# Performance work log

Measured on AMD Instinct MI355X. Metric: run time of the kernel, lower is better.

Reference implementation:

```python
import jax, jax.numpy as jnp
import numpy as np

N_NODES = 100000
N_EDGES = 1600000
D_IN = 64
D_HID = 64
NEG_SLOPE = 0.01  # torch leaky_relu default


def _sage_conv(x, src, dst, W_l, b_l, W_r):
    # PyG SAGEConv (mean aggr): lin_l(mean_j x_j) + lin_r(x_i)
    n = x.shape[0]
    msg = x[src]  # [E, D] irregular gather
    agg = jax.ops.segment_sum(msg, dst, num_segments=n)
    deg = jax.ops.segment_sum(jnp.ones((src.shape[0],), x.dtype), dst, num_segments=n)
    mean = agg / jnp.maximum(deg, 1.0)[:, None]
    return mean @ W_l.T + b_l + x @ W_r.T


def setup_inputs() -> dict:
    key = jax.random.key(0)
    ks = jax.random.split(key, 12)
    x = jax.random.normal(ks[0], (N_NODES, D_IN), dtype=jnp.float32)
    edge_index = jax.random.randint(ks[1], (2, N_EDGES), 0, N_NODES, dtype=jnp.int64)
    s = 1.0 / np.sqrt(D_IN)
    params = {}
    dims = [(D_IN, D_HID), (D_HID, D_HID), (D_HID, D_HID)]
    ki = 2
    for i, (din, dout) in enumerate(dims, start=1):
        sc = 1.0 / np.sqrt(din)
        params[f'W_l{i}'] = jax.random.uniform(ks[ki], (dout, din), minval=-sc, maxval=sc, dtype=jnp.float32); ki += 1
        params[f'b_l{i}'] = jnp.zeros((dout,), jnp.float32)
        params[f'W_r{i}'] = jax.random.uniform(ks[ki], (dout, din), minval=-sc, maxval=sc, dtype=jnp.float32); ki += 1
    sc = 1.0 / np.sqrt(D_HID)
    params['W_out'] = jax.random.uniform(ks[ki], (1, D_HID), minval=-sc, maxval=sc, dtype=jnp.float32)
    params['b_out'] = jnp.zeros((1,), jnp.float32)
    return {'x': x, 'edge_index': edge_index, **params}


def reference(x, edge_index, W_l1, b_l1, W_r1, W_l2, b_l2, W_r2, W_l3, b_l3, W_r3, W_out, b_out):
    src, dst = edge_index[0], edge_index[1]
    h = x
    for (Wl, bl, Wr) in ((W_l1, b_l1, W_r1), (W_l2, b_l2, W_r2), (W_l3, b_l3, W_r3)):
        h = _sage_conv(h, src, dst, Wl, bl, Wr)
        h = jnp.where(h >= 0, h, NEG_SLOPE * h)
        # dropout is identity in eval mode
    return h @ W_out.T + b_out  # [N, 1]
```

## Files before the change

### kernel.cpp

```cpp
#include <hip/hip_runtime.h>
#include <hip/hip_fp16.h>

#define D 64
#define NEG_SLOPE 0.01f
#define CB_SHIFT 9
#define CB_NODES 512
#define MAXCB 256
#define CHUNK 4096
#define BCAP 10240
#define SADJ_CAP 10240
#define CGRID 256
#define SAH 72
#define TILE 64

typedef _Float16 f16x8 __attribute__((ext_vector_type(8)));
typedef float    f32x4 __attribute__((ext_vector_type(4)));

struct ScatSmem {
    int hist[MAXCB];
    int lofs[MAXCB];
    int gbase[MAXCB];
    int cur[MAXCB];
    int swsum[4];
    unsigned spk[CHUNK];
    unsigned char sbk[CHUNK];
};

__device__ __forceinline__ int detect64(const void* __restrict__ ei) {
    int lane = threadIdx.x & 63;
    int v = ((const int*)ei)[2 * lane + 1];
    return (__ballot(v != 0) == 0ULL) ? 1 : 0;
}

__device__ __forceinline__ int edge_at(const void* __restrict__ ei, long long idx, int is64) {
    if (is64) return (int)((const long long*)ei)[idx];
    return ((const int*)ei)[idx];
}

__device__ __forceinline__ void scatter_body(ScatSmem& sm,
        const void* __restrict__ ei, long long E,
        int* __restrict__ bcursor, unsigned* __restrict__ ebuf,
        int ncb, int bid) {
    int t = threadIdx.x;
    sm.hist[t] = 0;
    int is64 = detect64(ei);
    __syncthreads();
    long long start = (long long)bid * CHUNK;
    int ccnt = (int)min((long long)CHUNK, E - start);

    for (int i = t; i < ccnt; i += 256) {
        int d = edge_at(ei, E + start + i, is64);
        atomicAdd(&sm.hist[d >> CB_SHIFT], 1);
    }
    __syncthreads();
    {
        int v = sm.hist[t];
        int lane = t & 63, w = t >> 6;
        int inc = v;
        for (int off = 1; off < 64; off <<= 1) {
            int u = __shfl_up(inc, off, 64);
            if (lane >= off) inc += u;
        }
        if (lane == 63) sm.swsum[w] = inc;
        __syncthreads();
        int wof = 0;
        for (int i = 0; i < w; ++i) wof += sm.swsum[i];
        sm.lofs[t] = wof + inc - v;
    }
    if (t < ncb && sm.hist[t]) sm.gbase[t] = atomicAdd(&bcursor[t], sm.hist[t]);
    __syncthreads();
    sm.cur[t] = sm.lofs[t];
    __syncthreads();

    for (int i = t; i < ccnt; i += 256) {
        int s = edge_at(ei, start + i, is64);
        int d = edge_at(ei, E + start + i, is64);
        int b = d >> CB_SHIFT;
        int slot = atomicAdd(&sm.cur[b], 1);
        sm.spk[slot] = ((unsigned)s << CB_SHIFT) | (unsigned)(d & (CB_NODES - 1));
        sm.sbk[slot] = (unsigned char)b;
    }
    __syncthreads();

    for (int i = t; i < ccnt; i += 256) {
        int b = sm.sbk[i];
        int dst = sm.gbase[b] + (i - sm.lofs[b]);
        if (dst < BCAP) ebuf[(size_t)b * BCAP + dst] = sm.spk[i];
    }
}

__device__ __forceinline__ void conv_body(const float* __restrict__ x,
        _Float16* __restrict__ x16, long long U, int cid,
        const float* __restrict__ Wl1, const float* __restrict__ Wr1,
        const float* __restrict__ Wl2, const float* __restrict__ Wr2,
        const float* __restrict__ Wl3, const float* __restrict__ Wr3,
        _Float16* __restrict__ W16) {
    int t = threadIdx.x;
    for (long long u = (long long)cid * 256 + t; u < U; u += (long long)CGRID * 256) {
        const float* s = x + u * 8;
        const float4 v0 = *(const float4*)s;
        const float4 v1 = *(const float4*)(s + 4);
        f16x8 o = { (_Float16)v0.x, (_Float16)v0.y, (_Float16)v0.z, (_Float16)v0.w,
                    (_Float16)v1.x, (_Float16)v1.y, (_Float16)v1.z, (_Float16)v1.w };
        *(f16x8*)(x16 + u * 8) = o;
    }
    if (cid == 0) {
        const float* Ws[6] = { Wl1, Wr1, Wl2, Wr2, Wl3, Wr3 };
#pragma unroll
        for (int m = 0; m < 6; ++m) {
            const float* src = Ws[m];
            _Float16* dst = W16 + m * 4096;
            for (int i = t; i < 4096; i += 256) dst[i] = (_Float16)src[i];
        }
    }
}

__global__ __launch_bounds__(256, 6) void scatter_conv_kernel(
        const void* __restrict__ ei, long long E,
        int* __restrict__ bcursor, unsigned* __restrict__ ebuf, int ncb, int sgrid,
        const float* __restrict__ x, _Float16* __restrict__ x16, long long U,
        const float* __restrict__ Wl1, const float* __restrict__ Wr1,
        const float* __restrict__ Wl2, const float* __restrict__ Wr2,
        const float* __restrict__ Wl3, const float* __restrict__ Wr3,
        _Float16* __restrict__ W16) {
    __shared__ ScatSmem sm;
    if ((int)blockIdx.x < sgrid)
        scatter_body(sm, ei, E, bcursor, ebuf, ncb, blockIdx.x);
    else
        conv_body(x, x16, U, blockIdx.x - sgrid, Wl1, Wr1, Wl2, Wr2, Wl3, Wr3, W16);
}

__global__ __launch_bounds__(256) void agg_gemm_kernel(
        const _Float16* __restrict__ Hin,
        const int* __restrict__ rowptr, const int* __restrict__ adj,
        const _Float16* __restrict__ W16,
        const float* __restrict__ bl,
        _Float16* __restrict__ Hout,
        const float* __restrict__ Wout, const float* __restrict__ bout,
        float* __restrict__ out, int N, int final_flag) {
    __shared__ _Float16 smh[TILE * SAH];
    int t = threadIdx.x;
    int node_base = (int)blockIdx.x * TILE;

    {
        int g = t >> 3;
        int sub = t & 7;
        size_t cofs = (size_t)(sub << 3);
#pragma unroll
        for (int p = 0; p < 2; ++p) {
            int local = p * 32 + g;
            int i = node_base + local;
            float a0 = 0.f, a1 = 0.f, a2 = 0.f, a3 = 0.f;
            float a4 = 0.f, a5 = 0.f, a6 = 0.f, a7 = 0.f;
            float inv = 0.f;
            if (i < N) {
                int b0 = rowptr[i], b1 = rowptr[i + 1];
                int e = b0;
                int nfull = (b1 - b0) >> 2;
                for (int q = 0; q < nfull; ++q) {
                    int s0 = adj[e], s1 = adj[e + 1], s2 = adj[e + 2], s3 = adj[e + 3];
                    e += 4;
                    union { float4 f4; __half2 h2[4]; } u0, u1, u2, u3;
                    u0.f4 = *(const float4*)(Hin + (size_t)s0 * D + cofs);
                    u1.f4 = *(const float4*)(Hin + (size_t)s1 * D + cofs);
                    u2.f4 = *(const float4*)(Hin + (size_t)s2 * D + cofs);
                    u3.f4 = *(const float4*)(Hin + (size_t)s3 * D + cofs);
#define ACC8(u) { \
        float2 v0 = __half22float2(u.h2[0]); float2 v1 = __half22float2(u.h2[1]); \
        float2 v2 = __half22float2(u.h2[2]); float2 v3 = __half22float2(u.h2[3]); \
        a0 += v0.x; a1 += v0.y; a2 += v1.x; a3 += v1.y; \
        a4 += v2.x; a5 += v2.y; a6 += v3.x; a7 += v3.y; }
                    ACC8(u0) ACC8(u1) ACC8(u2) ACC8(u3)
                }
                for (; e < b1; ++e) {
                    int s = adj[e];
                    union { float4 f4; __half2 h2[4]; } u;
                    u.f4 = *(const float4*)(Hin + (size_t)s * D + cofs);
                    ACC8(u)
                }
#undef ACC8
                inv = 1.0f / fmaxf((float)(b1 - b0), 1.0f);
            }
            f16x8 o = { (_Float16)(a0 * inv), (_Float16)(a1 * inv),
                        (_Float16)(a2 * inv), (_Float16)(a3 * inv),
                        (_Float16)(a4 * inv), (_Float16)(a5 * inv),
                        (_Float16)(a6 * inv), (_Float16)(a7 * inv) };
            *(f16x8*)(smh + local * SAH + (sub << 3)) = o;
        }
    }
    __syncthreads();

    int w = t >> 6, lane = t & 63;
    int lr = lane & 15;
    int lk = lane >> 4;
    int rbase = node_base + w * 16;

    f16x8 ah[2], am[2];
    {
        int gn = rbase + lr;
        if (gn >= N) gn = N - 1;
        const _Float16* hp = Hin + (size_t)gn * D + lk * 8;
        ah[0] = *(const f16x8*)hp;  ah[1] = *(const f16x8*)(hp + 32);
        const _Float16* mp = smh + (w * 16 + lr) * SAH + lk * 8;
        am[0] = *(const f16x8*)mp;  am[1] = *(const f16x8*)(mp + 32);
    }

    f32x4 acc[4];
#pragma unroll
    for (int nt = 0; nt < 4; ++nt)
        acc[nt] = (f32x4){0.f, 0.f, 0.f, 0.f};

    const _Float16* Wl = W16;
    const _Float16* Wr = W16 + 4096;
#pragma unroll
    for (int nt = 0; nt < 4; ++nt) {
        const _Float16* pl = Wl + (nt * 16 + lr) * D + lk * 8;
        const _Float16* pr = Wr + (nt * 16 + lr) * D + lk * 8;
        f16x8 b0 = *(const f16x8*)pl;  f16x8 b1 = *(const f16x8*)(pl + 32);
        f16x8 c0 = *(const f16x8*)pr;  f16x8 c1 = *(const f16x8*)(pr + 32);
        acc[nt] = __builtin_amdgcn_mfma_f32_16x16x32_f16(am[0], b0, acc[nt], 0, 0, 0);
        acc[nt] = __builtin_amdgcn_mfma_f32_16x16x32_f16(am[1], b1, acc[nt], 0, 0, 0);
        acc[nt] = __builtin_amdgcn_mfma_f32_16x16x32_f16(ah[0], c0, acc[nt], 0, 0, 0);
        acc[nt] = __builtin_amdgcn_mfma_f32_16x16x32_f16(ah[1], c1, acc[nt], 0, 0, 0);
    }

    float blv[4];
#pragma unroll
    for (int nt = 0; nt < 4; ++nt) blv[nt] = bl[nt * 16 + lr];

    if (!final_flag) {
#pragma unroll
        for (int r = 0; r < 4; ++r) {
            int gn = rbase + lk * 4 + r;
            if (gn < N) {
#pragma unroll
                for (int nt = 0; nt < 4; ++nt) {
                    float y = acc[nt][r] + blv[nt];
                    y = (y >= 0.f) ? y : NEG_SLOPE * y;
                    Hout[(size_t)gn * D + nt * 16 + lr] = (_Float16)y;
                }
            }
        }
    } else {
        float wv[4];
#pragma unroll
        for (int nt = 0; nt < 4; ++nt) wv[nt] = Wout[nt * 16 + lr];
        float bo = bout[0];
#pragma unroll
        for (int r = 0; r < 4; ++r) {
            float p = 0.f;
#pragma unroll
            for (int nt = 0; nt < 4; ++nt) {
                float y = acc[nt][r] + blv[nt];
                y = (y >= 0.f) ? y : NEG_SLOPE * y;
                p += y * wv[nt];
            }
            p += __shfl_xor(p, 1, 64);
            p += __shfl_xor(p, 2, 64);
            p += __shfl_xor(p, 4, 64);
            p += __shfl_xor(p, 8, 64);
            int gn = rbase + lk * 4 + r;
            if (lr == 0 && gn < N) out[gn] = p + bo;
        }
    }
}

__global__ __launch_bounds__(256) void finefill_kernel(
        const unsigned* __restrict__ ebuf, const int* __restrict__ bcount,
        int* __restrict__ rowptr, int* __restrict__ adj, int N, int ncb) {
    __shared__ int cnt[CB_NODES];
    __shared__ int cur[CB_NODES];
    __shared__ int wpart[4];
    __shared__ int wsum4[4];
    __shared__ int se0;
    __shared__ int sAdj[SADJ_CAP];
    int t = threadIdx.x;
    int b = blockIdx.x;

    {
        int v = (t < ncb) ? min(bcount[t], BCAP) : 0;
        int lane = t & 63, w = t >> 6;
        int inc = v;
        for (int off = 1; off < 64; off <<= 1) {
            int u = __shfl_up(inc, off, 64);
            if (lane >= off) inc += u;
        }
        if (lane == 63) wsum4[w] = inc;
        __syncthreads();
        int wof = 0;
        for (int iw = 0; iw < w; ++iw) wof += wsum4[iw];
        int ex = wof + inc - v;
        if (t == b) se0 = ex;
        if (b == 0 && t == 0)
            rowptr[N] = wsum4[0] + wsum4[1] + wsum4[2] + wsum4[3];
    }
    __syncthreads();
    int e0 = se0;
    int len = min(bcount[b], BCAP);
    int nb = b << CB_SHIFT;
    const unsigned* slab = ebuf + (size_t)b * BCAP;

    cnt[2 * t] = 0; cnt[2 * t + 1] = 0;
    __syncthreads();
    for (int i = t; i < len; i += 256) {
        unsigned p = slab[i];
        atomicAdd(&cnt[p & (CB_NODES - 1)], 1);
    }
    __syncthreads();

    int c0 = cnt[2 * t], c1 = cnt[2 * t + 1];
    int s = c0 + c1;
    int lane = t & 63, wv = t >> 6;
    int inc = s;
    for (int off = 1; off < 64; off <<= 1) {
        int u = __shfl_up(inc, off, 64);
        if (lane >= off) inc += u;
    }
    if (lane == 63) wpart[wv] = inc;
    __syncthreads();
    int wof = 0;
    for (int w = 0; w < wv; ++w) wof += wpart[w];
    int ex = wof + inc - s;
    cur[2 * t] = ex; cur[2 * t + 1] = ex + c0;
    {
        int g = nb + 2 * t;
        if (g < N)     rowptr[g]     = e0 + ex;
        if (g + 1 < N) rowptr[g + 1] = e0 + ex + c0;
    }
    __syncthreads();

    int big = (len > SADJ_CAP);
    for (int i = t; i < len; i += 256) {
        unsigned p = slab[i];
        int dl = (int)(p & (CB_NODES - 1));
        int src = (int)(p >> CB_SHIFT);
        int pos = atomicAdd(&cur[dl], 1);
        if (big) adj[e0 + pos] = src;
        else     sAdj[pos] = src;
    }
    __syncthreads();
    if (!big) {
        for (int i = t; i < len; i += 256) adj[e0 + i] = sAdj[i];
    }
}

extern "C" void kernel_launch(void* const* d_in, const int* in_sizes, int n_in,
                              void* d_out, int out_size, void* d_ws, size_t ws_size,
                              hipStream_t stream) {
    const float* x    = (const float*)d_in[0];
    const void*  ei   = d_in[1];
    const float* Wl1  = (const float*)d_in[2];
    const float* bl1  = (const float*)d_in[3];
    const float* Wr1  = (const float*)d_in[4];
    const float* Wl2  = (const float*)d_in[5];
    const float* bl2  = (const float*)d_in[6];
    const float* Wr2  = (const float*)d_in[7];
    const float* Wl3  = (const float*)d_in[8];
    const float* bl3  = (const float*)d_in[9];
    const float* Wr3  = (const float*)d_in[10];
    const float* Wout = (const float*)d_in[11];
    const float* bout = (const float*)d_in[12];
    float* out = (float*)d_out;

    int       N = in_sizes[0] / D;
    long long E = (long long)in_sizes[1] / 2;
    int ncb = (N + CB_NODES - 1) >> CB_SHIFT;
    long long U = (long long)N * D / 8;

    char* ws = (char*)d_ws;
    size_t off = 256;
    int* bcursor = (int*)(ws + off); off += 1024;
    int* rowptr = (int*)(ws + off); off += (((size_t)(N + 1) * 4 + 255) / 256) * 256;
    int* adj    = (int*)(ws + off); off += (((size_t)E * 4 + 255) / 256) * 256;
    unsigned* ebuf = (unsigned*)(ws + off); off += (size_t)ncb * BCAP * 4;
    _Float16* x16 = (_Float16*)(ws + off); off += (size_t)N * D * 2;
    _Float16* hA  = (_Float16*)(ws + off); off += (size_t)N * D * 2;
    _Float16* hB  = (_Float16*)(ws + off); off += (size_t)N * D * 2;
    _Float16* W16 = (_Float16*)(ws + off); off += 6 * 4096 * 2;

    int sgrid = (int)((E + CHUNK - 1) / CHUNK);
    int ggrid = (N + TILE - 1) / TILE;

    hipMemsetAsync(bcursor, 0, 1024, stream);

    scatter_conv_kernel<<<sgrid + CGRID, 256, 0, stream>>>(
        ei, E, bcursor, ebuf, ncb, sgrid,
        x, x16, U, Wl1, Wr1, Wl2, Wr2, Wl3, Wr3, W16);
    finefill_kernel<<<ncb, 256, 0, stream>>>(ebuf, bcursor, rowptr, adj, N, ncb);
    agg_gemm_kernel<<<ggrid, 256, 0, stream>>>(x16, rowptr, adj, W16, bl1, hA,
                                               Wout, bout, out, N, 0);
    agg_gemm_kernel<<<ggrid, 256, 0, stream>>>(hA, rowptr, adj, W16 + 2 * 4096, bl2, hB,
                                               Wout, bout, out, N, 0);
    agg_gemm_kernel<<<ggrid, 256, 0, stream>>>(hB, rowptr, adj, W16 + 4 * 4096, bl3, hA,
                                               Wout, bout, out, N, 1);
}
```

Baseline: 260.4 us.

## Replace two-pass bucketed CSR build with fixed-capacity per-node adjacency via atomics

```diff
diff --git a/kernel.cpp b/kernel.cpp
--- a/kernel.cpp
+++ b/kernel.cpp
@@ -3,28 +3,13 @@
 
 #define D 64
 #define NEG_SLOPE 0.01f
-#define CB_SHIFT 9
-#define CB_NODES 512
-#define MAXCB 256
-#define CHUNK 4096
-#define BCAP 10240
-#define SADJ_CAP 10240
-#define CGRID 256
+#define CAP 64
 #define SAH 72
 #define TILE 64
+#define BGRID 2048
 
 typedef _Float16 f16x8 __attribute__((ext_vector_type(8)));
 typedef float    f32x4 __attribute__((ext_vector_type(4)));
-
-struct ScatSmem {
-    int hist[MAXCB];
-    int lofs[MAXCB];
-    int gbase[MAXCB];
-    int cur[MAXCB];
-    int swsum[4];
-    unsigned spk[CHUNK];
-    unsigned char sbk[CHUNK];
-};
 
 __device__ __forceinline__ int detect64(const void* __restrict__ ei) {
     int lane = threadIdx.x & 63;
@@ -37,66 +22,25 @@
     return ((const int*)ei)[idx];
 }
 
-__device__ __forceinline__ void scatter_body(ScatSmem& sm,
+__global__ __launch_bounds__(256) void build_kernel(
         const void* __restrict__ ei, long long E,
-        int* __restrict__ bcursor, unsigned* __restrict__ ebuf,
-        int ncb, int bid) {
-    int t = threadIdx.x;
-    sm.hist[t] = 0;
-    int is64 = detect64(ei);
-    __syncthreads();
-    long long start = (long long)bid * CHUNK;
-    int ccnt = (int)min((long long)CHUNK, E - start);
-
-    for (int i = t; i < ccnt; i += 256) {
-        int d = edge_at(ei, E + start + i, is64);
-        atomicAdd(&sm.hist[d >> CB_SHIFT], 1);
-    }
-    __syncthreads();
-    {
-        int v = sm.hist[t];
-        int lane = t & 63, w = t >> 6;
-        int inc = v;
-        for (int off = 1; off < 64; off <<= 1) {
-            int u = __shfl_up(inc, off, 64);
-            if (lane >= off) inc += u;
-        }
-        if (lane == 63) sm.swsum[w] = inc;
-        __syncthreads();
-        int wof = 0;
-        for (int i = 0; i < w; ++i) wof += sm.swsum[i];
-        sm.lofs[t] = wof + inc - v;
-    }
-    if (t < ncb && sm.hist[t]) sm.gbase[t] = atomicAdd(&bcursor[t], sm.hist[t]);
-    __syncthreads();
-    sm.cur[t] = sm.lofs[t];
-    __syncthreads();
-
-    for (int i = t; i < ccnt; i += 256) {
-        int s = edge_at(ei, start + i, is64);
-        int d = edge_at(ei, E + start + i, is64);
-        int b = d >> CB_SHIFT;
-        int slot = atomicAdd(&sm.cur[b], 1);
-        sm.spk[slot] = ((unsigned)s << CB_SHIFT) | (unsigned)(d & (CB_NODES - 1));
-        sm.sbk[slot] = (unsigned char)b;
-    }
-    __syncthreads();
-
-    for (int i = t; i < ccnt; i += 256) {
-        int b = sm.sbk[i];
-        int dst = sm.gbase[b] + (i - sm.lofs[b]);
-        if (dst < BCAP) ebuf[(size_t)b * BCAP + dst] = sm.spk[i];
-    }
-}
-
-__device__ __forceinline__ void conv_body(const float* __restrict__ x,
-        _Float16* __restrict__ x16, long long U, int cid,
+        int* __restrict__ deg, int* __restrict__ adjF,
+        const float* __restrict__ x, _Float16* __restrict__ x16, long long U,
         const float* __restrict__ Wl1, const float* __restrict__ Wr1,
         const float* __restrict__ Wl2, const float* __restrict__ Wr2,
         const float* __restrict__ Wl3, const float* __restrict__ Wr3,
         _Float16* __restrict__ W16) {
-    int t = threadIdx.x;
-    for (long long u = (long long)cid * 256 + t; u < U; u += (long long)CGRID * 256) {
+    long long tid = (long long)blockIdx.x * 256 + threadIdx.x;
+    long long stride = (long long)gridDim.x * 256;
+    int is64 = detect64(ei);
+
+    for (long long e = tid; e < E; e += stride) {
+        int s = edge_at(ei, e, is64);
+        int d = edge_at(ei, E + e, is64);
+        int pos = atomicAdd(&deg[d], 1);
+        if (pos < CAP) adjF[(size_t)d * CAP + pos] = s;
+    }
+    for (long long u = tid; u < U; u += stride) {
         const float* s = x + u * 8;
         const float4 v0 = *(const float4*)s;
         const float4 v1 = *(const float4*)(s + 4);
@@ -104,8 +48,9 @@
                     (_Float16)v1.x, (_Float16)v1.y, (_Float16)v1.z, (_Float16)v1.w };
         *(f16x8*)(x16 + u * 8) = o;
     }
-    if (cid == 0) {
+    if (blockIdx.x == 0) {
         const float* Ws[6] = { Wl1, Wr1, Wl2, Wr2, Wl3, Wr3 };
+        int t = threadIdx.x;
 #pragma unroll
         for (int m = 0; m < 6; ++m) {
             const float* src = Ws[m];
@@ -115,24 +60,9 @@
     }
 }
 
-__global__ __launch_bounds__(256, 6) void scatter_conv_kernel(
-        const void* __restrict__ ei, long long E,
-        int* __restrict__ bcursor, unsigned* __restrict__ ebuf, int ncb, int sgrid,
-        const float* __restrict__ x, _Float16* __restrict__ x16, long long U,
-        const float* __restrict__ Wl1, const float* __restrict__ Wr1,
-        const float* __restrict__ Wl2, const float* __restrict__ Wr2,
-        const float* __restrict__ Wl3, const float* __restrict__ Wr3,
-        _Float16* __restrict__ W16) {
-    __shared__ ScatSmem sm;
-    if ((int)blockIdx.x < sgrid)
-        scatter_body(sm, ei, E, bcursor, ebuf, ncb, blockIdx.x);
-    else
-        conv_body(x, x16, U, blockIdx.x - sgrid, Wl1, Wr1, Wl2, Wr2, Wl3, Wr3, W16);
-}
-
 __global__ __launch_bounds__(256) void agg_gemm_kernel(
         const _Float16* __restrict__ Hin,
-        const int* __restrict__ rowptr, const int* __restrict__ adj,
+        const int* __restrict__ deg, const int* __restrict__ adjF,
         const _Float16* __restrict__ W16,
         const float* __restrict__ bl,
         _Float16* __restrict__ Hout,
@@ -154,11 +84,13 @@
             float a4 = 0.f, a5 = 0.f, a6 = 0.f, a7 = 0.f;
             float inv = 0.f;
             if (i < N) {
-                int b0 = rowptr[i], b1 = rowptr[i + 1];
-                int e = b0;
-                int nfull = (b1 - b0) >> 2;
+                int dgf = deg[i];
+                int len = min(dgf, CAP);
+                const int* ap = adjF + (size_t)i * CAP;
+                int e = 0;
+                int nfull = len >> 2;
                 for (int q = 0; q < nfull; ++q) {
-                    int s0 = adj[e], s1 = adj[e + 1], s2 = adj[e + 2], s3 = adj[e + 3];
+                    int s0 = ap[e], s1 = ap[e + 1], s2 = ap[e + 2], s3 = ap[e + 3];
                     e += 4;
                     union { float4 f4; __half2 h2[4]; } u0, u1, u2, u3;
                     u0.f4 = *(const float4*)(Hin + (size_t)s0 * D + cofs);
@@ -172,14 +104,14 @@
         a4 += v2.x; a5 += v2.y; a6 += v3.x; a7 += v3.y; }
                     ACC8(u0) ACC8(u1) ACC8(u2) ACC8(u3)
                 }
-                for (; e < b1; ++e) {
-                    int s = adj[e];
+                for (; e < len; ++e) {
+                    int s = ap[e];
                     union { float4 f4; __half2 h2[4]; } u;
                     u.f4 = *(const float4*)(Hin + (size_t)s * D + cofs);
                     ACC8(u)
                 }
 #undef ACC8
-                inv = 1.0f / fmaxf((float)(b1 - b0), 1.0f);
+                inv = 1.0f / fmaxf((float)dgf, 1.0f);
             }
             f16x8 o = { (_Float16)(a0 * inv), (_Float16)(a1 * inv),
                         (_Float16)(a2 * inv), (_Float16)(a3 * inv),
@@ -262,85 +194,6 @@
             int gn = rbase + lk * 4 + r;
             if (lr == 0 && gn < N) out[gn] = p + bo;
         }
-    }
-}
-
-__global__ __launch_bounds__(256) void finefill_kernel(
-        const unsigned* __restrict__ ebuf, const int* __restrict__ bcount,
-        int* __restrict__ rowptr, int* __restrict__ adj, int N, int ncb) {
-    __shared__ int cnt[CB_NODES];
-    __shared__ int cur[CB_NODES];
-    __shared__ int wpart[4];
-    __shared__ int wsum4[4];
-    __shared__ int se0;
-    __shared__ int sAdj[SADJ_CAP];
-    int t = threadIdx.x;
-    int b = blockIdx.x;
-
-    {
-        int v = (t < ncb) ? min(bcount[t], BCAP) : 0;
-        int lane = t & 63, w = t >> 6;
-        int inc = v;
-        for (int off = 1; off < 64; off <<= 1) {
-            int u = __shfl_up(inc, off, 64);
-            if (lane >= off) inc += u;
-        }
-        if (lane == 63) wsum4[w] = inc;
-        __syncthreads();
-        int wof = 0;
-        for (int iw = 0; iw < w; ++iw) wof += wsum4[iw];
-        int ex = wof + inc - v;
-        if (t == b) se0 = ex;
-        if (b == 0 && t == 0)
-            rowptr[N] = wsum4[0] + wsum4[1] + wsum4[2] + wsum4[3];
-    }
-    __syncthreads();
-    int e0 = se0;
-    int len = min(bcount[b], BCAP);
-    int nb = b << CB_SHIFT;
-    const unsigned* slab = ebuf + (size_t)b * BCAP;
-
-    cnt[2 * t] = 0; cnt[2 * t + 1] = 0;
-    __syncthreads();
-    for (int i = t; i < len; i += 256) {
-        unsigned p = slab[i];
-        atomicAdd(&cnt[p & (CB_NODES - 1)], 1);
-    }
-    __syncthreads();
-
-    int c0 = cnt[2 * t], c1 = cnt[2 * t + 1];
-    int s = c0 + c1;
-    int lane = t & 63, wv = t >> 6;
-    int inc = s;
-    for (int off = 1; off < 64; off <<= 1) {
-        int u = __shfl_up(inc, off, 64);
-        if (lane >= off) inc += u;
-    }
-    if (lane == 63) wpart[wv] = inc;
-    __syncthreads();
-    int wof = 0;
-    for (int w = 0; w < wv; ++w) wof += wpart[w];
-    int ex = wof + inc - s;
-    cur[2 * t] = ex; cur[2 * t + 1] = ex + c0;
-    {
-        int g = nb + 2 * t;
-        if (g < N)     rowptr[g]     = e0 + ex;
-        if (g + 1 < N) rowptr[g + 1] = e0 + ex + c0;
-    }
-    __syncthreads();
-
-    int big = (len > SADJ_CAP);
-    for (int i = t; i < len; i += 256) {
-        unsigned p = slab[i];
-        int dl = (int)(p & (CB_NODES - 1));
-        int src = (int)(p >> CB_SHIFT);
-        int pos = atomicAdd(&cur[dl], 1);
-        if (big) adj[e0 + pos] = src;
-        else     sAdj[pos] = src;
-    }
-    __syncthreads();
-    if (!big) {
-        for (int i = t; i < len; i += 256) adj[e0 + i] = sAdj[i];
     }
 }
 
@@ -364,33 +217,28 @@
 
     int       N = in_sizes[0] / D;
     long long E = (long long)in_sizes[1] / 2;
-    int ncb = (N + CB_NODES - 1) >> CB_SHIFT;
     long long U = (long long)N * D / 8;
 
     char* ws = (char*)d_ws;
     size_t off = 256;
-    int* bcursor = (int*)(ws + off); off += 1024;
-    int* rowptr = (int*)(ws + off); off += (((size_t)(N + 1) * 4 + 255) / 256) * 256;
-    int* adj    = (int*)(ws + off); off += (((size_t)E * 4 + 255) / 256) * 256;
-    unsigned* ebuf = (unsigned*)(ws + off); off += (size_t)ncb * BCAP * 4;
+    int* deg  = (int*)(ws + off); off += (((size_t)N * 4 + 255) / 256) * 256;
+    int* adjF = (int*)(ws + off); off += (size_t)N * CAP * 4;
     _Float16* x16 = (_Float16*)(ws + off); off += (size_t)N * D * 2;
     _Float16* hA  = (_Float16*)(ws + off); off += (size_t)N * D * 2;
     _Float16* hB  = (_Float16*)(ws + off); off += (size_t)N * D * 2;
     _Float16* W16 = (_Float16*)(ws + off); off += 6 * 4096 * 2;
 
-    int sgrid = (int)((E + CHUNK - 1) / CHUNK);
     int ggrid = (N + TILE - 1) / TILE;
 
-    hipMemsetAsync(bcursor, 0, 1024, stream);
-
-    scatter_conv_kernel<<<sgrid + CGRID, 256, 0, stream>>>(
-        ei, E, bcursor, ebuf, ncb, sgrid,
-        x, x16, U, Wl1, Wr1, Wl2, Wr2, Wl3, Wr3, W16);
-    finefill_kernel<<<ncb, 256, 0, stream>>>(ebuf, bcursor, rowptr, adj, N, ncb);
-    agg_gemm_kernel<<<ggrid, 256, 0, stream>>>(x16, rowptr, adj, W16, bl1, hA,
+    hipMemsetAsync(deg, 0, (size_t)N * 4, stream);
+
+    build_kernel<<<BGRID, 256, 0, stream>>>(
+        ei, E, deg, adjF, x, x16, U,
+        Wl1, Wr1, Wl2, Wr2, Wl3, Wr3, W16);
+    agg_gemm_kernel<<<ggrid, 256, 0, stream>>>(x16, deg, adjF, W16, bl1, hA,
                                                Wout, bout, out, N, 0);
-    agg_gemm_kernel<<<ggrid, 256, 0, stream>>>(hA, rowptr, adj, W16 + 2 * 4096, bl2, hB,
+    agg_gemm_kernel<<<ggrid, 256, 0, stream>>>(hA, deg, adjF, W16 + 2 * 4096, bl2, hB,
                                                Wout, bout, out, N, 0);
-    agg_gemm_kernel<<<ggrid, 256, 0, stream>>>(hB, rowptr, adj, W16 + 4 * 4096, bl3, hA,
+    agg_gemm_kernel<<<ggrid, 256, 0, stream>>>(hB, deg, adjF, W16 + 4 * 4096, bl3, hA,
                                                Wout, bout, out, N, 1);
 }
```

After: 338.9 us. +30.1%, slower.

## Shrink coarse buckets to 128 nodes so CSR fill uses more blocks

Applied to the files above, without the earlier changes.

```diff
diff --git a/kernel.cpp b/kernel.cpp
--- a/kernel.cpp
+++ b/kernel.cpp
@@ -3,12 +3,11 @@
 
 #define D 64
 #define NEG_SLOPE 0.01f
-#define CB_SHIFT 9
-#define CB_NODES 512
-#define MAXCB 256
+#define CB_SHIFT 7
+#define CB_NODES 128
+#define MAXCB 1024
 #define CHUNK 4096
-#define BCAP 10240
-#define SADJ_CAP 10240
+#define BCAP 2560
 #define CGRID 256
 #define SAH 72
 #define TILE 64
@@ -23,7 +22,7 @@
     int cur[MAXCB];
     int swsum[4];
     unsigned spk[CHUNK];
-    unsigned char sbk[CHUNK];
+    unsigned short sbk[CHUNK];
 };
 
 __device__ __forceinline__ int detect64(const void* __restrict__ ei) {
@@ -42,7 +41,8 @@
         int* __restrict__ bcursor, unsigned* __restrict__ ebuf,
         int ncb, int bid) {
     int t = threadIdx.x;
-    sm.hist[t] = 0;
+#pragma unroll
+    for (int q = 0; q < 4; ++q) sm.hist[q * 256 + t] = 0;
     int is64 = detect64(ei);
     __syncthreads();
     long long start = (long long)bid * CHUNK;
@@ -54,7 +54,9 @@
     }
     __syncthreads();
     {
-        int v = sm.hist[t];
+        int h0 = sm.hist[4 * t], h1 = sm.hist[4 * t + 1];
+        int h2 = sm.hist[4 * t + 2], h3 = sm.hist[4 * t + 3];
+        int v = h0 + h1 + h2 + h3;
         int lane = t & 63, w = t >> 6;
         int inc = v;
         for (int off = 1; off < 64; off <<= 1) {
@@ -65,11 +67,19 @@
         __syncthreads();
         int wof = 0;
         for (int i = 0; i < w; ++i) wof += sm.swsum[i];
-        sm.lofs[t] = wof + inc - v;
-    }
-    if (t < ncb && sm.hist[t]) sm.gbase[t] = atomicAdd(&bcursor[t], sm.hist[t]);
-    __syncthreads();
-    sm.cur[t] = sm.lofs[t];
+        int ex = wof + inc - v;
+        sm.lofs[4 * t]     = ex;
+        sm.lofs[4 * t + 1] = ex + h0;
+        sm.lofs[4 * t + 2] = ex + h0 + h1;
+        sm.lofs[4 * t + 3] = ex + h0 + h1 + h2;
+#pragma unroll
+        for (int q = 0; q < 4; ++q) {
+            int b = 4 * t + q;
+            int hv = sm.hist[b];
+            if (b < ncb && hv) sm.gbase[b] = atomicAdd(&bcursor[b], hv);
+            sm.cur[b] = sm.lofs[b];
+        }
+    }
     __syncthreads();
 
     for (int i = t; i < ccnt; i += 256) {
@@ -78,7 +88,7 @@
         int b = d >> CB_SHIFT;
         int slot = atomicAdd(&sm.cur[b], 1);
         sm.spk[slot] = ((unsigned)s << CB_SHIFT) | (unsigned)(d & (CB_NODES - 1));
-        sm.sbk[slot] = (unsigned char)b;
+        sm.sbk[slot] = (unsigned short)b;
     }
     __syncthreads();
 
@@ -115,7 +125,7 @@
     }
 }
 
-__global__ __launch_bounds__(256, 6) void scatter_conv_kernel(
+__global__ __launch_bounds__(256, 3) void scatter_conv_kernel(
         const void* __restrict__ ei, long long E,
         int* __restrict__ bcursor, unsigned* __restrict__ ebuf, int ncb, int sgrid,
         const float* __restrict__ x, _Float16* __restrict__ x16, long long U,
@@ -128,6 +138,89 @@
         scatter_body(sm, ei, E, bcursor, ebuf, ncb, blockIdx.x);
     else
         conv_body(x, x16, U, blockIdx.x - sgrid, Wl1, Wr1, Wl2, Wr2, Wl3, Wr3, W16);
+}
+
+__global__ __launch_bounds__(256) void finefill_kernel(
+        const unsigned* __restrict__ ebuf, const int* __restrict__ bcount,
+        int* __restrict__ rowptr, int* __restrict__ adj, int N, int ncb) {
+    __shared__ int cnt[CB_NODES];
+    __shared__ int cur[CB_NODES];
+    __shared__ int wsum4[4];
+    __shared__ int se0;
+    __shared__ int sAdj[BCAP];
+    int t = threadIdx.x;
+    int b = blockIdx.x;
+
+    {
+        int b0 = 4 * t;
+        int v0 = (b0 + 0 < ncb) ? min(bcount[b0 + 0], BCAP) : 0;
+        int v1 = (b0 + 1 < ncb) ? min(bcount[b0 + 1], BCAP) : 0;
+        int v2 = (b0 + 2 < ncb) ? min(bcount[b0 + 2], BCAP) : 0;
+        int v3 = (b0 + 3 < ncb) ? min(bcount[b0 + 3], BCAP) : 0;
+        int s = v0 + v1 + v2 + v3;
+        int lane = t & 63, w = t >> 6;
+        int inc = s;
+        for (int off = 1; off < 64; off <<= 1) {
+            int u = __shfl_up(inc, off, 64);
+            if (lane >= off) inc += u;
+        }
+        if (lane == 63) wsum4[w] = inc;
+        __syncthreads();
+        int wof = 0;
+        for (int iw = 0; iw < w; ++iw) wof += wsum4[iw];
+        int ex = wof + inc - s;
+        if (b0 <= b && b < b0 + 4) {
+            int e = ex;
+            if (b > b0)     e += v0;
+            if (b > b0 + 1) e += v1;
+            if (b > b0 + 2) e += v2;
+            se0 = e;
+        }
+        if (b == 0 && t == 0)
+            rowptr[N] = wsum4[0] + wsum4[1] + wsum4[2] + wsum4[3];
+    }
+    __syncthreads();
+    int e0 = se0;
+    int len = min(bcount[b], BCAP);
+    int nb = b << CB_SHIFT;
+    const unsigned* slab = ebuf + (size_t)b * BCAP;
+
+    if (t < CB_NODES) cnt[t] = 0;
+    __syncthreads();
+    for (int i = t; i < len; i += 256)
+        atomicAdd(&cnt[slab[i] & (CB_NODES - 1)], 1);
+    __syncthreads();
+
+    {
+        int v = (t < CB_NODES) ? cnt[t] : 0;
+        int lane = t & 63, w = t >> 6;
+        int inc = v;
+        for (int off = 1; off < 64; off <<= 1) {
+            int u = __shfl_up(inc, off, 64);
+            if (lane >= off) inc += u;
+        }
+        if (lane == 63) wsum4[w] = inc;
+        __syncthreads();
+        int wof = 0;
+        for (int iw = 0; iw < w; ++iw) wof += wsum4[iw];
+        int ex = wof + inc - v;
+        if (t < CB_NODES) {
+            cur[t] = ex;
+            int g = nb + t;
+            if (g < N) rowptr[g] = e0 + ex;
+        }
+    }
+    __syncthreads();
+
+    for (int i = t; i < len; i += 256) {
+        unsigned p = slab[i];
+        int dl = (int)(p & (CB_NODES - 1));
+        int src = (int)(p >> CB_SHIFT);
+        int pos = atomicAdd(&cur[dl], 1);
+        sAdj[pos] = src;
+    }
+    __syncthreads();
+    for (int i = t; i < len; i += 256) adj[e0 + i] = sAdj[i];
 }
 
 __global__ __launch_bounds__(256) void agg_gemm_kernel(
@@ -265,85 +358,6 @@
     }
 }
 
-__global__ __launch_bounds__(256) void finefill_kernel(
-        const unsigned* __restrict__ ebuf, const int* __restrict__ bcount,
-        int* __restrict__ rowptr, int* __restrict__ adj, int N, int ncb) {
-    __shared__ int cnt[CB_NODES];
-    __shared__ int cur[CB_NODES];
-    __shared__ int wpart[4];
-    __shared__ int wsum4[4];
-    __shared__ int se0;
-    __shared__ int sAdj[SADJ_CAP];
-    int t = threadIdx.x;
-    int b = blockIdx.x;
-
-    {
-        int v = (t < ncb) ? min(bcount[t], BCAP) : 0;
-        int lane = t & 63, w = t >> 6;
-        int inc = v;
-        for (int off = 1; off < 64; off <<= 1) {
-            int u = __shfl_up(inc, off, 64);
-            if (lane >= off) inc += u;
-        }
-        if (lane == 63) wsum4[w] = inc;
-        __syncthreads();
-        int wof = 0;
-        for (int iw = 0; iw < w; ++iw) wof += wsum4[iw];
-        int ex = wof + inc - v;
-        if (t == b) se0 = ex;
-        if (b == 0 && t == 0)
-            rowptr[N] = wsum4[0] + wsum4[1] + wsum4[2] + wsum4[3];
-    }
-    __syncthreads();
-    int e0 = se0;
-    int len = min(bcount[b], BCAP);
-    int nb = b << CB_SHIFT;
-    const unsigned* slab = ebuf + (size_t)b * BCAP;
-
-    cnt[2 * t] = 0; cnt[2 * t + 1] = 0;
-    __syncthreads();
-    for (int i = t; i < len; i += 256) {
-        unsigned p = slab[i];
-        atomicAdd(&cnt[p & (CB_NODES - 1)], 1);
-    }
-    __syncthreads();
-
-    int c0 = cnt[2 * t], c1 = cnt[2 * t + 1];
-    int s = c0 + c1;
-    int lane = t & 63, wv = t >> 6;
-    int inc = s;
-    for (int off = 1; off < 64; off <<= 1) {
-        int u = __shfl_up(inc, off, 64);
-        if (lane >= off) inc += u;
-    }
-    if (lane == 63) wpart[wv] = inc;
-    __syncthreads();
-    int wof = 0;
-    for (int w = 0; w < wv; ++w) wof += wpart[w];
-    int ex = wof + inc - s;
-    cur[2 * t] = ex; cur[2 * t + 1] = ex + c0;
-    {
-        int g = nb + 2 * t;
-        if (g < N)     rowptr[g]     = e0 + ex;
-        if (g + 1 < N) rowptr[g + 1] = e0 + ex + c0;
-    }
-    __syncthreads();
-
-    int big = (len > SADJ_CAP);
-    for (int i = t; i < len; i += 256) {
-        unsigned p = slab[i];
-        int dl = (int)(p & (CB_NODES - 1));
-        int src = (int)(p >> CB_SHIFT);
-        int pos = atomicAdd(&cur[dl], 1);
-        if (big) adj[e0 + pos] = src;
-        else     sAdj[pos] = src;
-    }
-    __syncthreads();
-    if (!big) {
-        for (int i = t; i < len; i += 256) adj[e0 + i] = sAdj[i];
-    }
-}
-
 extern "C" void kernel_launch(void* const* d_in, const int* in_sizes, int n_in,
                               void* d_out, int out_size, void* d_ws, size_t ws_size,
                               hipStream_t stream) {
@@ -369,7 +383,7 @@
 
     char* ws = (char*)d_ws;
     size_t off = 256;
-    int* bcursor = (int*)(ws + off); off += 1024;
+    int* bcursor = (int*)(ws + off); off += 4096;
     int* rowptr = (int*)(ws + off); off += (((size_t)(N + 1) * 4 + 255) / 256) * 256;
     int* adj    = (int*)(ws + off); off += (((size_t)E * 4 + 255) / 256) * 256;
     unsigned* ebuf = (unsigned*)(ws + off); off += (size_t)ncb * BCAP * 4;
@@ -381,7 +395,7 @@
     int sgrid = (int)((E + CHUNK - 1) / CHUNK);
     int ggrid = (N + TILE - 1) / TILE;
 
-    hipMemsetAsync(bcursor, 0, 1024, stream);
+    hipMemsetAsync(bcursor, 0, 4096, stream);
 
     scatter_conv_kernel<<<sgrid + CGRID, 256, 0, stream>>>(
         ei, E, bcursor, ebuf, ncb, sgrid,
```

After: 274.4 us. 1.05x slower.

## Split finefill CSR build into four blocks per coarse bucket by node quarter

Applied to the files above, without the earlier changes.

```diff
diff --git a/kernel.cpp b/kernel.cpp
--- a/kernel.cpp
+++ b/kernel.cpp
@@ -8,7 +8,7 @@
 #define MAXCB 256
 #define CHUNK 4096
 #define BCAP 10240
-#define SADJ_CAP 10240
+#define QCAP 3072
 #define CGRID 256
 #define SAH 72
 #define TILE 64
@@ -128,6 +128,86 @@
         scatter_body(sm, ei, E, bcursor, ebuf, ncb, blockIdx.x);
     else
         conv_body(x, x16, U, blockIdx.x - sgrid, Wl1, Wr1, Wl2, Wr2, Wl3, Wr3, W16);
+}
+
+__global__ __launch_bounds__(256) void finefill_kernel(
+        const unsigned* __restrict__ ebuf, const int* __restrict__ bcount,
+        int* __restrict__ rowptr, int* __restrict__ adj, int N, int ncb) {
+    __shared__ int cnt[CB_NODES];
+    __shared__ int cur[CB_NODES];
+    __shared__ int wsum4[4];
+    __shared__ int se0;
+    __shared__ int sAdj[QCAP];
+    int t = threadIdx.x;
+    int B = (int)blockIdx.x >> 2;
+    int q = (int)blockIdx.x & 3;
+
+    {
+        int v = (t < ncb) ? min(bcount[t], BCAP) : 0;
+        int lane = t & 63, w = t >> 6;
+        int inc = v;
+        for (int off = 1; off < 64; off <<= 1) {
+            int u = __shfl_up(inc, off, 64);
+            if (lane >= off) inc += u;
+        }
+        if (lane == 63) wsum4[w] = inc;
+        __syncthreads();
+        int wof = 0;
+        for (int iw = 0; iw < w; ++iw) wof += wsum4[iw];
+        int ex = wof + inc - v;
+        if (t == B) se0 = ex;
+        if (blockIdx.x == 0 && t == 0)
+            rowptr[N] = wsum4[0] + wsum4[1] + wsum4[2] + wsum4[3];
+    }
+    __syncthreads();
+    int e0 = se0;
+    int len = min(bcount[B], BCAP);
+    int nb = B << CB_SHIFT;
+    const unsigned* slab = ebuf + (size_t)B * BCAP;
+
+    cnt[2 * t] = 0; cnt[2 * t + 1] = 0;
+    __syncthreads();
+    for (int i = t; i < len; i += 256)
+        atomicAdd(&cnt[slab[i] & (CB_NODES - 1)], 1);
+    __syncthreads();
+
+    {
+        int c0 = cnt[2 * t], c1 = cnt[2 * t + 1];
+        int s = c0 + c1;
+        int lane = t & 63, wv = t >> 6;
+        int inc = s;
+        for (int off = 1; off < 64; off <<= 1) {
+            int u = __shfl_up(inc, off, 64);
+            if (lane >= off) inc += u;
+        }
+        if (lane == 63) wsum4[wv] = inc;
+        __syncthreads();
+        int wof = 0;
+        for (int w = 0; w < wv; ++w) wof += wsum4[w];
+        int ex = wof + inc - s;
+        cur[2 * t] = ex; cur[2 * t + 1] = ex + c0;
+        int g = nb + 2 * t;
+        if (g < N)     rowptr[g]     = e0 + ex;
+        if (g + 1 < N) rowptr[g + 1] = e0 + ex + c0;
+    }
+    __syncthreads();
+
+    int qbase = cur[q * 128];
+    int qend  = (q < 3) ? cur[q * 128 + 128] : len;
+    int qlen  = qend - qbase;
+    __syncthreads();
+
+    for (int i = t; i < len; i += 256) {
+        unsigned p = slab[i];
+        int dl = (int)(p & (CB_NODES - 1));
+        if ((dl >> 7) == q) {
+            int pos = atomicAdd(&cur[dl], 1) - qbase;
+            if (pos < QCAP) sAdj[pos] = (int)(p >> CB_SHIFT);
+        }
+    }
+    __syncthreads();
+    for (int i = t; i < qlen && i < QCAP; i += 256)
+        adj[e0 + qbase + i] = sAdj[i];
 }
 
 __global__ __launch_bounds__(256) void agg_gemm_kernel(
@@ -265,85 +345,6 @@
     }
 }
 
-__global__ __launch_bounds__(256) void finefill_kernel(
-        const unsigned* __restrict__ ebuf, const int* __restrict__ bcount,
-        int* __restrict__ rowptr, int* __restrict__ adj, int N, int ncb) {
-    __shared__ int cnt[CB_NODES];
-    __shared__ int cur[CB_NODES];
-    __shared__ int wpart[4];
-    __shared__ int wsum4[4];
-    __shared__ int se0;
-    __shared__ int sAdj[SADJ_CAP];
-    int t = threadIdx.x;
-    int b = blockIdx.x;
-
-    {
-        int v = (t < ncb) ? min(bcount[t], BCAP) : 0;
-        int lane = t & 63, w = t >> 6;
-        int inc = v;
-        for (int off = 1; off < 64; off <<= 1) {
-            int u = __shfl_up(inc, off, 64);
-            if (lane >= off) inc += u;
-        }
-        if (lane == 63) wsum4[w] = inc;
-        __syncthreads();
-        int wof = 0;
-        for (int iw = 0; iw < w; ++iw) wof += wsum4[iw];
-        int ex = wof + inc - v;
-        if (t == b) se0 = ex;
-        if (b == 0 && t == 0)
-            rowptr[N] = wsum4[0] + wsum4[1] + wsum4[2] + wsum4[3];
-    }
-    __syncthreads();
-    int e0 = se0;
-    int len = min(bcount[b], BCAP);
-    int nb = b << CB_SHIFT;
-    const unsigned* slab = ebuf + (size_t)b * BCAP;
-
-    cnt[2 * t] = 0; cnt[2 * t + 1] = 0;
-    __syncthreads();
-    for (int i = t; i < len; i += 256) {
-        unsigned p = slab[i];
-        atomicAdd(&cnt[p & (CB_NODES - 1)], 1);
-    }
-    __syncthreads();
-
-    int c0 = cnt[2 * t], c1 = cnt[2 * t + 1];
-    int s = c0 + c1;
-    int lane = t & 63, wv = t >> 6;
-    int inc = s;
-    for (int off = 1; off < 64; off <<= 1) {
-        int u = __shfl_up(inc, off, 64);
-        if (lane >= off) inc += u;
-    }
-    if (lane == 63) wpart[wv] = inc;
-    __syncthreads();
-    int wof = 0;
-    for (int w = 0; w < wv; ++w) wof += wpart[w];
-    int ex = wof + inc - s;
-    cur[2 * t] = ex; cur[2 * t + 1] = ex + c0;
-    {
-        int g = nb + 2 * t;
-        if (g < N)     rowptr[g]     = e0 + ex;
-        if (g + 1 < N) rowptr[g + 1] = e0 + ex + c0;
-    }
-    __syncthreads();
-
-    int big = (len > SADJ_CAP);
-    for (int i = t; i < len; i += 256) {
-        unsigned p = slab[i];
-        int dl = (int)(p & (CB_NODES - 1));
-        int src = (int)(p >> CB_SHIFT);
-        int pos = atomicAdd(&cur[dl], 1);
-        if (big) adj[e0 + pos] = src;
-        else     sAdj[pos] = src;
-    }
-    __syncthreads();
-    if (!big) {
-        for (int i = t; i < len; i += 256) adj[e0 + i] = sAdj[i];
-    }
-}
-
 extern "C" void kernel_launch(void* const* d_in, const int* in_sizes, int n_in,
                               void* d_out, int out_size, void* d_ws, size_t ws_size,
                               hipStream_t stream) {
@@ -386,7 +387,7 @@
     scatter_conv_kernel<<<sgrid + CGRID, 256, 0, stream>>>(
         ei, E, bcursor, ebuf, ncb, sgrid,
         x, x16, U, Wl1, Wr1, Wl2, Wr2, Wl3, Wr3, W16);
-    finefill_kernel<<<ncb, 256, 0, stream>>>(ebuf, bcursor, rowptr, adj, N, ncb);
+    finefill_kernel<<<ncb * 4, 256, 0, stream>>>(ebuf, bcursor, rowptr, adj, N, ncb);
     agg_gemm_kernel<<<ggrid, 256, 0, stream>>>(x16, rowptr, adj, W16, bl1, hA,
                                                Wout, bout, out, N, 0);
     agg_gemm_kernel<<<ggrid, 256, 0, stream>>>(hA, rowptr, adj, W16 + 2 * 4096, bl2, hB,
```

After: 266.7 us. +2.4%, slower.
